# Kernel tuning notes

Hardware: AMD Instinct MI355X
Metric: run time of the kernel (lower is better)

## Reference

```python
import jax, jax.numpy as jnp
import numpy as np

IMG = 224; P = 16; C_IN = 3; D = 768; DEPTH = 12; H = 12; HD = D // H
MLP = 4 * D; NCLS = 1000
GRID = IMG // P; NPATCH = GRID * GRID; N = NPATCH + 1
NRD = (2 * GRID - 1) * (2 * GRID - 1) + 3  # num_relative_distance


def _rel_pos_index():
    # replicates the torch buffer construction (BEiT-style)
    coords = np.stack(np.meshgrid(np.arange(GRID), np.arange(GRID), indexing='ij')).reshape(2, -1)
    rel = (coords[:, :, None] - coords[:, None, :]).transpose(1, 2, 0).astype(np.int64)
    rel[:, :, 0] += GRID - 1
    rel[:, :, 1] += GRID - 1
    rel[:, :, 0] *= 2 * GRID - 1
    idx = np.zeros((N, N), dtype=np.int64)
    idx[1:, 1:] = rel.sum(-1)
    idx[0, :] = NRD - 3
    idx[:, 0] = NRD - 2
    idx[0, 0] = NRD - 1
    return jnp.asarray(idx)

REL_IDX = _rel_pos_index()  # [N, N] int


def setup_inputs() -> dict:
    key = jax.random.key(0)
    ks = jax.random.split(key, 12)
    r = lambda k, shp: jax.random.normal(k, shp, jnp.float32) * 0.02
    return {
        'x': jax.random.normal(ks[0], (32, C_IN, IMG, IMG), jnp.float32),
        'patch_w': r(ks[1], (D, C_IN * P * P)),
        'patch_b': jnp.zeros((D,), jnp.float32),
        'cls_token': r(ks[2], (1, 1, D)),
        'pos_embed': r(ks[3], (1, N, D)),
        'norm1_s': jnp.ones((DEPTH, D), jnp.float32),
        'norm1_b': jnp.zeros((DEPTH, D), jnp.float32),
        'qkv_w': r(ks[4], (DEPTH, 3 * D, D)),
        'q_bias': jnp.zeros((DEPTH, D), jnp.float32),
        'v_bias': jnp.zeros((DEPTH, D), jnp.float32),
        'rpb_table': r(ks[5], (DEPTH, NRD, H)),
        'proj_w': r(ks[6], (DEPTH, D, D)),
        'proj_b': jnp.zeros((DEPTH, D), jnp.float32),
        'norm2_s': jnp.ones((DEPTH, D), jnp.float32),
        'norm2_b': jnp.zeros((DEPTH, D), jnp.float32),
        'fc1_w': r(ks[7], (DEPTH, MLP, D)),
        'fc1_b': jnp.zeros((DEPTH, MLP), jnp.float32),
        'fc2_w': r(ks[8], (DEPTH, D, MLP)),
        'fc2_b': jnp.zeros((DEPTH, D), jnp.float32),
        'gamma1': jnp.full((DEPTH, D), 0.1, jnp.float32),
        'gamma2': jnp.full((DEPTH, D), 0.1, jnp.float32),
        'normf_s': jnp.ones((D,), jnp.float32),
        'normf_b': jnp.zeros((D,), jnp.float32),
        'head_w': r(ks[9], (NCLS, D)),
        'head_b': jnp.zeros((NCLS,), jnp.float32),
    }


def _ln(x, s, b):
    m = jnp.mean(x, -1, keepdims=True)
    v = jnp.mean((x - m) ** 2, -1, keepdims=True)
    return (x - m) * jax.lax.rsqrt(v + 1e-5) * s + b


def reference(x, patch_w, patch_b, cls_token, pos_embed, norm1_s, norm1_b, qkv_w,
              q_bias, v_bias, rpb_table, proj_w, proj_b, norm2_s, norm2_b,
              fc1_w, fc1_b, fc2_w, fc2_b, gamma1, gamma2, normf_s, normf_b,
              head_w, head_b):
    B = x.shape[0]
    # Patch embed: stride=kernel conv == unfold + matmul
    t = x.reshape(B, C_IN, GRID, P, GRID, P).transpose(0, 2, 4, 1, 3, 5).reshape(B, NPATCH, C_IN * P * P)
    t = t @ patch_w.T + patch_b                                   # [B, 196, D]
    t = jnp.concatenate([jnp.broadcast_to(cls_token, (B, 1, D)), t], axis=1) + pos_embed
    scale = HD ** -0.5
    for i in range(DEPTH):
        h = _ln(t, norm1_s[i], norm1_b[i])
        qkv_b = jnp.concatenate([q_bias[i], jnp.zeros_like(q_bias[i]), v_bias[i]])
        qkv = (h @ qkv_w[i].T + qkv_b).reshape(B, N, 3, H, HD)
        q = qkv[:, :, 0].transpose(0, 2, 1, 3)                    # [B, H, N, HD]
        k = qkv[:, :, 1].transpose(0, 2, 1, 3)
        v = qkv[:, :, 2].transpose(0, 2, 1, 3)
        bias = rpb_table[i][REL_IDX].transpose(2, 0, 1)           # [H, N, N]
        attn = jax.nn.softmax(jnp.einsum('bhqd,bhkd->bhqk', q * scale, k) + bias[None], axis=-1)
        o = jnp.einsum('bhqk,bhkd->bhqd', attn, v).transpose(0, 2, 1, 3).reshape(B, N, D)
        t = t + gamma1[i] * (o @ proj_w[i].T + proj_b[i])
        h2 = _ln(t, norm2_s[i], norm2_b[i])
        m = jax.nn.gelu(h2 @ fc1_w[i].T + fc1_b[i], approximate=False) @ fc2_w[i].T + fc2_b[i]
        t = t + gamma2[i] * m
    t = _ln(t, normf_s, normf_b)
    return t[:, 0] @ head_w.T + head_b                            # [B, NCLS]
```

## Files before the change

### kernel.cpp

```cpp
#include <hip/hip_runtime.h>
#include <hip/hip_bf16.h>


typedef __hip_bfloat16 bf16s;
using bf16x8 = __attribute__((ext_vector_type(8))) __bf16;
using f32x4  = __attribute__((ext_vector_type(4))) float;

#define DEV static __device__ __forceinline__

DEV float b2f(bf16s x) { return __bfloat162float(x); }
DEV bf16s f2b(float x) { return __float2bfloat16(x); }

DEV void gload_lds16(const void* g, void* l) {
  __builtin_amdgcn_global_load_lds((const __attribute__((address_space(1))) void*)g,
                                   (__attribute__((address_space(3))) void*)l, 16, 0, 0);
}

constexpr int B_   = 32;
constexpr int H_   = 12;
constexpr int NTOK = 197;
constexpr int NPAD = 224;
constexpr int MVALP= 6272;
constexpr int MVAL = B_*NTOK;
constexpr int MROW = 6400;
constexpr int MLP_ = 3072;
constexpr int BH   = B_*H_;
constexpr int NRD  = 732;
constexpr int NNP  = 7*32*16*14;

constexpr size_t OFF_T   = 0;
constexpr size_t SZ_T    = (size_t)MROW*768*4;
constexpr size_t OFF_H   = OFF_T + SZ_T;
constexpr size_t SZ_H    = (size_t)MROW*768*2;
constexpr size_t OFF_Q   = OFF_H + SZ_H;
constexpr size_t SZ_QKB  = (size_t)BH*NPAD*64*2;
constexpr size_t OFF_K   = OFF_Q + SZ_QKB;
constexpr size_t OFF_VT  = OFF_K + SZ_QKB;
constexpr size_t OFF_P   = OFF_VT + SZ_QKB;
constexpr size_t SZ_P    = (size_t)MROW*MLP_*2;
constexpr size_t OFF_O   = OFF_P + SZ_P;
constexpr size_t OFF_BT  = OFF_O + SZ_H;
constexpr size_t SZ_BT   = (size_t)12*H_*NNP*2;
constexpr size_t OFF_HF  = OFF_BT + SZ_BT;
constexpr size_t OFF_WB  = OFF_HF + 49152;
constexpr size_t WS_NEED = OFF_WB + (size_t)7077888*2;

constexpr size_t WB_QKV = 0;
constexpr size_t WB_PROJ= (size_t)2304*768;
constexpr size_t WB_FC1 = WB_PROJ + (size_t)768*768;
constexpr size_t WB_FC2 = WB_FC1 + (size_t)MLP_*768;

template<int MODE>
__global__ __launch_bounds__(512, 4)
void gemm8p(const bf16s* __restrict__ A, const bf16s* __restrict__ Bw,
            const int K, const int ldc,
            bf16s* __restrict__ Cb,
            const float* __restrict__ e0, const float* __restrict__ e1,
            float* __restrict__ tres,
            bf16s* __restrict__ qp, bf16s* __restrict__ kp, bf16s* __restrict__ vp)
{
  __shared__ bf16s lds[32768];
  const int tid  = threadIdx.x;
  const int lane = tid & 63;
  const int wid  = tid >> 6;
  const int wm   = wid >> 2, wn = wid & 3;

  const int ncols = gridDim.y;
  const int nwg = (int)gridDim.x * ncols;
  const int lin = (int)blockIdx.y * gridDim.x + blockIdx.x;
  const int xcd = lin & 7, pos = lin >> 3;
  const int q8 = nwg >> 3, r8 = nwg & 7;
  const int vid = (xcd < r8) ? xcd*(q8+1) + pos : r8*(q8+1) + (xcd-r8)*q8 + pos;
  constexpr int NBG = (MODE == 0) ? 6 : 8;
  const int gsz = NBG * (int)gridDim.x;
  const int g   = vid / gsz;
  const int rr  = vid - g*gsz;
  const int bm  = rr / NBG;
  const int bn  = g*NBG + (rr - bm*NBG);

  const int srow = (wid << 3) + (lane >> 3);
  const int colg = (((lane & 7) ^ (srow & 7)) << 3);
  const bf16s* gA = A  + (size_t)(bm*128 + srow)*K + colg;
  const bf16s* gB = Bw + (size_t)(bn*128 + srow)*K + colg;
  const size_t rK64 = (size_t)64*K;

  const int r15  = lane & 15;
  const int colr = (lane >> 4) << 3;
  const int exor = (lane & 7) << 3;
  const int ardA = wm*4096 + r15*64;
  const int ardB = 8192 + (wn*32 + r15)*64;

  f32x4 acc[4][2] = {};
  const int J = K >> 7;

#define STGA(h, kt, dbuf) do { \
    const bf16s* _g = gA + (size_t)(h)*rK64 + (size_t)(kt)*64; \
    gload_lds16(_g, &lds[(dbuf)*16384 + (h)*4096 + wid*512 + lane*8]); } while(0)
#define STGB(h, kt, dbuf) do { \
    const bf16s* _g = gB + (size_t)(h)*rK64 + (size_t)(kt)*64; \
    gload_lds16(_g, &lds[(dbuf)*16384 + 8192 + (h)*4096 + wid*512 + lane*8]); } while(0)

  STGB(0,0,0); STGB(1,0,0);
  STGA(0,0,0); STGA(1,0,0);
  STGB(0,1,1); STGB(1,1,1);

  bf16x8 bfr[2][2];

  for (int j = 0; j < J; ++j) {
    const bool more = (j+1 < J);
#pragma unroll
    for (int p = 0; p < 4; ++p) {
      __builtin_amdgcn_sched_barrier(0);
      if (p == 0) {
        asm volatile("s_waitcnt vmcnt(2)" ::: "memory");
      } else if (p == 2) {
        if (j+1 == J) asm volatile("s_waitcnt vmcnt(0)" ::: "memory");
        else          asm volatile("s_waitcnt vmcnt(2)" ::: "memory");
      }
      __builtin_amdgcn_sched_barrier(0);
      __builtin_amdgcn_s_barrier();
      __builtin_amdgcn_sched_barrier(0);

      if (p == 0)      { STGA(0, 2*j+1, 1); STGA(1, 2*j+1, 1); }
      else if (p == 1) { if (more) { STGB(0, 2*j+2, 0); STGB(1, 2*j+2, 0); } }
      else if (p == 2) { if (more) { STGA(0, 2*j+2, 0); STGA(1, 2*j+2, 0); } }
      else             { if (more) { STGB(0, 2*j+3, 1); STGB(1, 2*j+3, 1); } }

      const int d = (p < 2) ? 0 : 1;
      const int dbase = d*16384;
      const int q0 = (p & 1) << 1;
      if ((p & 1) == 0) {
#pragma unroll
        for (int nf=0; nf<2; nf++)
#pragma unroll
          for (int kss=0; kss<2; kss++)
            bfr[nf][kss] = *(const bf16x8*)&lds[dbase + ardB + nf*1024 + (((kss<<5) + colr) ^ exor)];
      }
      bf16x8 a1[2][2];
#pragma unroll
      for (int qq=0; qq<2; qq++)
#pragma unroll
        for (int kss=0; kss<2; kss++)
          a1[qq][kss] = *(const bf16x8*)&lds[dbase + ardA + (q0+qq)*1024 + (((kss<<5) + colr) ^ exor)];
      __builtin_amdgcn_s_setprio(1);
#pragma unroll
      for (int qq=0; qq<2; qq++)
#pragma unroll
        for (int nf=0; nf<2; nf++)
#pragma unroll
          for (int kss=0; kss<2; kss++)
            acc[q0+qq][nf] = __builtin_amdgcn_mfma_f32_16x16x32_bf16(a1[qq][kss], bfr[nf][kss], acc[q0+qq][nf], 0, 0, 0);
      __builtin_amdgcn_s_setprio(0);
    }
  }
#undef STGA
#undef STGB

  const int crow0 = (lane >> 4) * 4;

  if (MODE == 5) {
    __syncthreads();
#pragma unroll
    for (int mf = 0; mf < 4; ++mf)
#pragma unroll
      for (int nf = 0; nf < 2; ++nf)
#pragma unroll
        for (int r = 0; r < 4; ++r) {
          const int lrow = wm*64 + mf*16 + crow0 + r;
          const int lcol = wn*32 + nf*16 + r15;
          const float xx = acc[mf][nf][r] + e0[bn*128 + lcol];
          lds[lrow*136 + lcol] = f2b(0.5f*xx*(1.0f + erff(xx*0.70710678118654752f)));
        }
    __syncthreads();
#pragma unroll
    for (int it = 0; it < 4; ++it) {
      const int sid = it*512 + tid;
      const int row = sid >> 4, cg = sid & 15;
      const int grow = bm*128 + row;
      *(uint4*)&Cb[(size_t)grow*ldc + bn*128 + cg*8] =
          *(const uint4*)&lds[row*136 + cg*8];
    }
    return;
  }

  if (MODE == 0 && bn >= 12) {
    float* lf = (float*)lds;
    __syncthreads();
#pragma unroll
    for (int mf = 0; mf < 4; ++mf)
#pragma unroll
      for (int nf = 0; nf < 2; ++nf)
#pragma unroll
        for (int r = 0; r < 4; ++r) {
          const int col = wn*32 + nf*16 + r15;
          const int row = wm*64 + mf*16 + crow0 + r;
          lf[col*128 + (row ^ (col & 31))] = acc[mf][nf][r];
        }
    __syncthreads();
    const int rem0 = bn*128 - 1536;
#pragma unroll
    for (int ci = 0; ci < 16; ++ci) {
      const int c = wid*16 + ci;
      const int rem = rem0 + c;
      const int hh = rem >> 6, dd = rem & 63;
      const float vb = e1[rem];
      bf16s* vrow = vp + ((size_t)hh*64 + dd)*NPAD;
#pragma unroll
      for (int hf2 = 0; hf2 < 2; ++hf2) {
        const int row = hf2*64 + lane;
        const int grow = bm*128 + row;
        if (grow < MVAL) {
          const int b2 = grow/197, ntok = grow - b2*197;
          vrow[(size_t)b2*H_*64*NPAD + ntok] = f2b(lf[c*128 + (row ^ (c & 31))] + vb);
        }
      }
    }
    return;
  }

  if (MODE == 0) {
    const bool isq = (bn < 6);
    __syncthreads();
#pragma unroll
    for (int mf = 0; mf < 4; ++mf)
#pragma unroll
      for (int nf = 0; nf < 2; ++nf)
#pragma unroll
        for (int r = 0; r < 4; ++r) {
          const int lrow = wm*64 + mf*16 + crow0 + r;
          const int lcol = wn*32 + nf*16 + r15;
          float v = acc[mf][nf][r];
          if (isq) v = (v + e0[bn*128 + lcol])*0.125f;
          lds[lrow*136 + lcol] = f2b(v);
        }
    __syncthreads();
    bf16s* outp = isq ? qp : kp;
#pragma unroll
    for (int it = 0; it < 4; ++it) {
      const int sid = it*512 + tid;
      const int row = sid >> 4, cg = sid & 15;
      const int grow = bm*128 + row;
      if (grow < MVAL) {
        const int bb_ = grow/197, ntok = grow - bb_*197;
        const int lcol = cg*8;
        const int rem = isq ? (bn*128 + lcol) : (bn*128 + lcol - 768);
        const int hh = rem >> 6, dd = rem & 63;
        *(uint4*)&outp[(((size_t)bb_*H_ + hh)*NPAD + ntok)*64 + dd] =
            *(const uint4*)&lds[row*136 + lcol];
      }
    }
  }
}

template<int MODE>
__global__ __launch_bounds__(256, 3)
void gemm64n(const bf16s* __restrict__ A, const bf16s* __restrict__ Bw,
             const int K, const int ldc, bf16s* __restrict__ Cb,
             const float* __restrict__ e0, const float* __restrict__ e1,
             float* __restrict__ tres)
{
  __shared__ bf16s lds[24576];
  const int tid  = threadIdx.x;
  const int lane = tid & 63;
  const int wid  = tid >> 6;
  const int wm   = wid >> 1, wn = wid & 1;

  const int ncols = gridDim.y;
  const int nwg = (int)gridDim.x * ncols;
  const int lin = (int)blockIdx.y * gridDim.x + blockIdx.x;
  const int xcd = lin & 7, pos = lin >> 3;
  const int q8 = nwg >> 3, r8 = nwg & 7;
  const int vid = (xcd < r8) ? xcd*(q8+1) + pos : r8*(q8+1) + (xcd-r8)*q8 + pos;
  const int bm = vid / ncols, bn = vid - bm*ncols;

  const int srow = tid >> 3;
  const int colg = (((tid & 7) ^ (srow & 7)) << 3);
  const bf16s* gA = A  + (size_t)(bm*128 + srow)*K + colg;
  const bf16s* gB = Bw + (size_t)(bn*64  + srow)*K + colg;
  const size_t rK32 = (size_t)32*K;

  const int r15  = lane & 15;
  const int colr = (lane >> 4) << 3;
  const int exor = (lane & 7) << 3;
  const int ardA = wm*4096 + r15*64;
  const int ardB = 8192 + (wn*32 + r15)*64;

  f32x4 acc[4][2] = {};
  const int J = K >> 7;

#define STGA2(h, kt, dbuf) do { \
    const bf16s* _g = gA + (size_t)(h)*rK32 + (size_t)(kt)*64; \
    gload_lds16(_g, &lds[(dbuf)*12288 + (h)*2048 + tid*8]); } while(0)
#define STGB2(h, kt, dbuf) do { \
    const bf16s* _g = gB + (size_t)(h)*rK32 + (size_t)(kt)*64; \
    gload_lds16(_g, &lds[(dbuf)*12288 + 8192 + (h)*2048 + tid*8]); } while(0)

  STGB2(0,0,0); STGB2(1,0,0);
  STGA2(0,0,0); STGA2(1,0,0); STGA2(2,0,0); STGA2(3,0,0);
  STGB2(0,1,1); STGB2(1,1,1);

  bf16x8 bfr[2][2];

  for (int j = 0; j < J; ++j) {
    const bool more = (j+1 < J);
#pragma unroll
    for (int p = 0; p < 4; ++p) {
      __builtin_amdgcn_sched_barrier(0);
      if (p == 0) {
        asm volatile("s_waitcnt vmcnt(2)" ::: "memory");
      } else if (p == 2) {
        if (j+1 == J) asm volatile("s_waitcnt vmcnt(0)" ::: "memory");
        else          asm volatile("s_waitcnt vmcnt(2)" ::: "memory");
      }
      __builtin_amdgcn_sched_barrier(0);
      __builtin_amdgcn_s_barrier();
      __builtin_amdgcn_sched_barrier(0);

      if (p == 0)      { STGA2(0, 2*j+1, 1); STGA2(1, 2*j+1, 1); STGA2(2, 2*j+1, 1); STGA2(3, 2*j+1, 1); }
      else if (p == 1) { if (more) { STGB2(0, 2*j+2, 0); STGB2(1, 2*j+2, 0); } }
      else if (p == 2) { if (more) { STGA2(0, 2*j+2, 0); STGA2(1, 2*j+2, 0); STGA2(2, 2*j+2, 0); STGA2(3, 2*j+2, 0); } }
      else             { if (more) { STGB2(0, 2*j+3, 1); STGB2(1, 2*j+3, 1); } }

      const int d = (p < 2) ? 0 : 1;
      const int dbase = d*12288;
      const int q0 = (p & 1) << 1;
      if ((p & 1) == 0) {
#pragma unroll
        for (int nf=0; nf<2; nf++)
#pragma unroll
          for (int kss=0; kss<2; kss++)
            bfr[nf][kss] = *(const bf16x8*)&lds[dbase + ardB + nf*1024 + (((kss<<5) + colr) ^ exor)];
      }
      bf16x8 a1[2][2];
#pragma unroll
      for (int qq=0; qq<2; qq++)
#pragma unroll
        for (int kss=0; kss<2; kss++)
          a1[qq][kss] = *(const bf16x8*)&lds[dbase + ardA + (q0+qq)*1024 + (((kss<<5) + colr) ^ exor)];
      __builtin_amdgcn_s_setprio(1);
#pragma unroll
      for (int qq=0; qq<2; qq++)
#pragma unroll
        for (int nf=0; nf<2; nf++)
#pragma unroll
          for (int kss=0; kss<2; kss++)
            acc[q0+qq][nf] = __builtin_amdgcn_mfma_f32_16x16x32_bf16(a1[qq][kss], bfr[nf][kss], acc[q0+qq][nf], 0, 0, 0);
      __builtin_amdgcn_s_setprio(0);
    }
  }
#undef STGA2
#undef STGB2

  const int crow0 = (lane >> 4) * 4;
#pragma unroll
  for (int mf = 0; mf < 4; ++mf) {
#pragma unroll
    for (int r = 0; r < 4; ++r) {
      const int grow = bm*128 + wm*64 + mf*16 + crow0 + r;
      {
        float* trow = tres + (size_t)grow*768;
#pragma unroll
        for (int nf = 0; nf < 2; ++nf) {
          const int gcol = bn*64 + wn*32 + nf*16 + r15;
          trow[gcol] += e1[gcol]*(acc[mf][nf][r] + e0[gcol]);
        }
      }
    }
  }
}

__global__ __launch_bounds__(256, 5)
void gemm64p(const bf16s* __restrict__ A, const bf16s* __restrict__ Bw,
             int K,
             const float* __restrict__ e0, const float* __restrict__ e1,
             float* __restrict__ tres)
{
  __shared__ bf16s As[2][64*32];
  __shared__ bf16s Bs[2][128*32];
  const int tid  = threadIdx.x;
  const int lane = tid & 63;
  const int wave = tid >> 6;

  const int ncols = gridDim.y;
  const int nwg = (int)gridDim.x * ncols;
  const int lin = (int)blockIdx.y * gridDim.x + blockIdx.x;
  const int xcd = lin & 7, pos = lin >> 3;
  const int q8 = nwg >> 3, r8 = nwg & 7;
  const int vid = (xcd < r8) ? xcd*(q8+1) + pos : r8*(q8+1) + (xcd-r8)*q8 + pos;
  const int bm = vid / ncols, bn = vid - bm*ncols;

  f32x4 acc[2][4] = {};

  const int sr4  = lane >> 2;
  const int scol = ((lane&3) ^ (sr4&3))*8;
  const bf16s* gA = A  + (size_t)(bm*64  + wave*16 + sr4)*K + scol;
  const bf16s* gB = Bw + (size_t)(bn*128 + wave*32 + sr4)*K + scol;
  const size_t b16 = (size_t)16*K;
  const int dA  = wave*512  + lane*8;
  const int dB0 = wave*1024 + lane*8, dB1 = dB0 + 512;

  const int fr  = lane & 15;
  const int rdk = (((lane>>4) ^ (lane&3)))*8;
  const int wr = wave >> 1, wc = wave & 1;
  const int abase = (wr*32 + fr)*32 + rdk;
  const int bbase = (wc*64 + fr)*32 + rdk;

  const int nk = K >> 5;
  gload_lds16(gA,       &As[0][dA]);
  gload_lds16(gB,       &Bs[0][dB0]);
  gload_lds16(gB + b16, &Bs[0][dB1]);

  int cur = 0;
  for (int kt = 0; kt < nk; ++kt) {
    __syncthreads();
    if (kt + 1 < nk) {
      const bf16s* ga = gA + (size_t)(kt+1)*32;
      const bf16s* gb = gB + (size_t)(kt+1)*32;
      gload_lds16(ga,       &As[cur^1][dA]);
      gload_lds16(gb,       &Bs[cur^1][dB0]);
      gload_lds16(gb + b16, &Bs[cur^1][dB1]);
    }
    bf16x8 af[2], bfr[4];
    af[0] = *(const bf16x8*)&As[cur][abase];
    af[1] = *(const bf16x8*)&As[cur][abase + 512];
#pragma unroll
    for (int n2=0;n2<4;n2++) bfr[n2] = *(const bf16x8*)&Bs[cur][bbase + n2*512];
#pragma unroll
    for (int m=0;m<2;m++)
#pragma unroll
      for (int n2=0;n2<4;n2++)
        acc[m][n2] = __builtin_amdgcn_mfma_f32_16x16x32_bf16(af[m], bfr[n2], acc[m][n2], 0, 0, 0);
    cur ^= 1;
  }

  const int crow0 = (lane>>4)*4;
#pragma unroll
  for (int m=0;m<2;m++) {
#pragma unroll
    for (int r=0;r<4;r++) {
      const int grow = bm*64 + wr*32 + m*16 + crow0 + r;
      if (grow >= MVALP) continue;
      const int bb_ = grow/196, p = grow - bb_*196;
      float* trow = tres + ((size_t)bb_*197 + 1 + p)*768;
      const float* prow = e1 + (size_t)(1+p)*768;
#pragma unroll
      for (int n2=0;n2<4;n2++) {
        const int gcol = bn*128 + wc*64 + n2*16 + fr;
        trow[gcol] = acc[m][n2][r] + e0[gcol] + prow[gcol];
      }
    }
  }
}

__global__ __launch_bounds__(256)
void f2b_k(const float* __restrict__ src, bf16s* __restrict__ dst, int n4)
{
  int id = blockIdx.x*256 + threadIdx.x;
  if (id >= n4) return;
  const float4 v = ((const float4*)src)[id];
  union { bf16s b[4]; uint2 u; } uu;
  uu.b[0] = f2b(v.x); uu.b[1] = f2b(v.y); uu.b[2] = f2b(v.z); uu.b[3] = f2b(v.w);
  ((uint2*)dst)[id] = uu.u;
}

__global__ __launch_bounds__(256)
void prep_k(const float* __restrict__ tin, const float* __restrict__ s,
            const float* __restrict__ b, bf16s* __restrict__ outp,
            const float* __restrict__ qw, const float* __restrict__ pw,
            const float* __restrict__ f1, const float* __restrict__ f2,
            bf16s* __restrict__ wb)
{
  const int tid = threadIdx.x;
  if (blockIdx.x < MVAL) {
    const int r = blockIdx.x;
    const float* xr = tin + (size_t)r*768;
    float v0 = xr[tid], v1 = xr[tid+256], v2 = xr[tid+512];
    float sum = v0+v1+v2;
#pragma unroll
    for (int off=32; off>=1; off>>=1) sum += __shfl_xor(sum, off, 64);
    __shared__ float red[8];
    const int wv = tid>>6, ln = tid&63;
    if (ln==0) red[wv] = sum;
    __syncthreads();
    const float mean = (red[0]+red[1]+red[2]+red[3]) * (1.0f/768.0f);
    const float d0=v0-mean, d1=v1-mean, d2=v2-mean;
    float sq = d0*d0 + d1*d1 + d2*d2;
#pragma unroll
    for (int off=32; off>=1; off>>=1) sq += __shfl_xor(sq, off, 64);
    if (ln==0) red[4+wv] = sq;
    __syncthreads();
    const float rs = rsqrtf((red[4]+red[5]+red[6]+red[7])*(1.0f/768.0f) + 1e-5f);
    bf16s* orow = outp + (size_t)r*768;
    orow[tid]     = f2b(d0*rs*s[tid]     + b[tid]);
    orow[tid+256] = f2b(d1*rs*s[tid+256] + b[tid+256]);
    orow[tid+512] = f2b(d2*rs*s[tid+512] + b[tid+512]);
  } else {
    int id = (blockIdx.x - MVAL)*256 + tid;
    const float* src; size_t dst; int loc;
    if (id < 442368)           { src = qw; loc = id;          dst = WB_QKV; }
    else if (id < 589824)      { src = pw; loc = id-442368;   dst = WB_PROJ; }
    else if (id < 1179648)     { src = f1; loc = id-589824;   dst = WB_FC1; }
    else                       { src = f2; loc = id-1179648;  dst = WB_FC2; }
    const float4 v = ((const float4*)src)[loc];
    union { bf16s bb[4]; uint2 u; } uu;
    uu.bb[0] = f2b(v.x); uu.bb[1] = f2b(v.y); uu.bb[2] = f2b(v.z); uu.bb[3] = f2b(v.w);
    ((uint2*)(wb + dst))[loc] = uu.u;
  }
}

__global__ __launch_bounds__(256)
void bias_all_k(const float* __restrict__ rpb, bf16s* __restrict__ biasT)
{
  int id = blockIdx.x*256 + threadIdx.x;
  if (id >= 12*H_*NNP) return;
  const int l   = id / (H_*NNP);
  const int r2  = id - l*(H_*NNP);
  const int hh  = r2 / NNP;
  const int rem = r2 - hh*NNP;
  const int qt   = rem / 7168;
  const int idx2 = rem - qt*7168;
  const int lrow = idx2 / 224;
  const int idx3 = idx2 - lrow*224;
  const int fr   = idx3 / 14;
  const int nt   = idx3 - fr*14;
  int i = qt*32 + lrow;
  int j = nt*16 + fr;
  if (i > 196) i = 196;
  if (j > 196) j = 196;
  int v;
  if (i==0 && j==0)      v = NRD-1;
  else if (i==0)         v = NRD-3;
  else if (j==0)         v = NRD-2;
  else {
    const int p = i-1, q = j-1;
    v = (p/14 - q/14 + 13)*27 + (p%14 - q%14 + 13);
  }
  biasT[id] = f2b(rpb[(size_t)l*NRD*H_ + v*H_ + hh]);
}

__global__ __launch_bounds__(256)
void im2col_k(const float* __restrict__ x, bf16s* __restrict__ pat)
{
  int id = blockIdx.x*256 + threadIdx.x;
  if (id >= MVALP*768) return;
  int col = id % 768;  int row = id / 768;
  int b = row / 196, p = row % 196;
  int gy = p / 14, gx = p % 14;
  int c = col >> 8, rem = col & 255, py = rem >> 4, px = rem & 15;
  pat[id] = f2b(x[ ((size_t)(b*3 + c)*224 + gy*16 + py)*224 + gx*16 + px ]);
}

__global__ __launch_bounds__(256)
void clspos_k(const float* __restrict__ cls, const float* __restrict__ pos, float* __restrict__ t)
{
  int id = blockIdx.x*256 + threadIdx.x;
  int d = id % 768, b = id / 768;
  t[(size_t)b*197*768 + d] = cls[d] + pos[d];
}

__global__ __launch_bounds__(256)
void ln_k(const float* __restrict__ tin, const float* __restrict__ s,
          const float* __restrict__ b, bf16s* __restrict__ outp, int instride)
{
  const int r = blockIdx.x, tid = threadIdx.x;
  const float* xr = tin + (size_t)r*instride;
  float v0 = xr[tid], v1 = xr[tid+256], v2 = xr[tid+512];
  float sum = v0+v1+v2;
#pragma unroll
  for (int off=32; off>=1; off>>=1) sum += __shfl_xor(sum, off, 64);
  __shared__ float red[8];
  const int wv = tid>>6, ln = tid&63;
  if (ln==0) red[wv] = sum;
  __syncthreads();
  const float mean = (red[0]+red[1]+red[2]+red[3]) * (1.0f/768.0f);
  const float d0=v0-mean, d1=v1-mean, d2=v2-mean;
  float sq = d0*d0 + d1*d1 + d2*d2;
#pragma unroll
  for (int off=32; off>=1; off>>=1) sq += __shfl_xor(sq, off, 64);
  if (ln==0) red[4+wv] = sq;
  __syncthreads();
  const float rs = rsqrtf((red[4]+red[5]+red[6]+red[7])*(1.0f/768.0f) + 1e-5f);
  bf16s* orow = outp + (size_t)r*768;
  orow[tid]     = f2b(d0*rs*s[tid]     + b[tid]);
  orow[tid+256] = f2b(d1*rs*s[tid+256] + b[tid+256]);
  orow[tid+512] = f2b(d2*rs*s[tid+512] + b[tid+512]);
}

__global__ __launch_bounds__(64)
void attn_fused(const bf16s* __restrict__ q, const bf16s* __restrict__ k,
                const bf16s* __restrict__ vT, const bf16s* __restrict__ biasT,
                bf16s* __restrict__ o)
{
  __shared__ bf16s Pl[32][232];
  bf16s* Plf = &Pl[0][0];
  const int gid = blockIdx.x;
  const int qt = gid % 7, bh = gid / 7;
  const int b = bh / H_, hh = bh % H_;
  const int lane = threadIdx.x;
  const int fr = lane & 15, fk = (lane>>4)*8;
  const int g4 = (lane >> 4) * 4;

  const bf16s* bTq = biasT + (size_t)hh*NNP + (size_t)qt*7168;
#pragma unroll
  for (int it = 0; it < 14; ++it)
    gload_lds16(bTq + it*512 + lane*8, &Plf[it*512 + lane*8]);

  const bf16s* qp = q + (size_t)bh*NPAD*64;
  const bf16s* kp = k + (size_t)bh*NPAD*64;
  bf16x8 a[2][2];
#pragma unroll
  for (int m=0;m<2;m++)
#pragma unroll
    for (int kk=0;kk<2;kk++)
      a[m][kk] = *(const bf16x8*)&qp[(qt*32 + m*16 + fr)*64 + kk*32 + fk];

  f32x4 acc[2][13] = {};
  __builtin_amdgcn_s_setprio(1);
#pragma unroll
  for (int nt=0; nt<13; nt++) {
    bf16x8 bb0 = *(const bf16x8*)&kp[(nt*16 + fr)*64 + fk];
    bf16x8 bb1 = *(const bf16x8*)&kp[(nt*16 + fr)*64 + 32 + fk];
    acc[0][nt] = __builtin_amdgcn_mfma_f32_16x16x32_bf16(a[0][0], bb0, acc[0][nt], 0,0,0);
    acc[0][nt] = __builtin_amdgcn_mfma_f32_16x16x32_bf16(a[0][1], bb1, acc[0][nt], 0,0,0);
    acc[1][nt] = __builtin_amdgcn_mfma_f32_16x16x32_bf16(a[1][0], bb0, acc[1][nt], 0,0,0);
    acc[1][nt] = __builtin_amdgcn_mfma_f32_16x16x32_bf16(a[1][1], bb1, acc[1][nt], 0,0,0);
  }
  __builtin_amdgcn_s_setprio(0);

  asm volatile("s_waitcnt vmcnt(0)" ::: "memory");
  __builtin_amdgcn_sched_barrier(0);

  const uint* Plu = (const uint*)Plf;
  const bf16s zb = f2b(0.0f);

#pragma unroll
  for (int mm = 0; mm < 2; ++mm) {
    const int m = 1 - mm;
    uint br[4][7];
#pragma unroll
    for (int r2 = 0; r2 < 4; ++r2) {
      const int lrow = m*16 + g4 + r2;
      const int ub = (lrow*224 + fr*14) >> 1;
#pragma unroll
      for (int j = 0; j < 7; ++j) br[r2][j] = Plu[ub + j];
    }
#pragma unroll
    for (int r2 = 0; r2 < 4; ++r2) {
      const int lrow = m*16 + g4 + r2;
      const int row = qt*32 + lrow;
      if (row < NTOK) {
        float s[13]; float mx = -3.0e38f;
#pragma unroll
        for (int nt = 0; nt < 12; ++nt) {
          const uint u = br[r2][nt >> 1];
          const uint bb = (nt & 1) ? (u & 0xffff0000u) : (u << 16);
          const float v = acc[m][nt][r2] + __uint_as_float(bb);
          s[nt] = v;
          mx = fmaxf(mx, v);
        }
        {
          const uint u = br[r2][6];
          const float v = acc[m][12][r2] + __uint_as_float(u << 16);
          s[12] = v;
          if (fr < 5) mx = fmaxf(mx, v);
        }
        mx = fmaxf(mx, __shfl_xor(mx, 1, 64));
        mx = fmaxf(mx, __shfl_xor(mx, 2, 64));
        mx = fmaxf(mx, __shfl_xor(mx, 4, 64));
        mx = fmaxf(mx, __shfl_xor(mx, 8, 64));
        float sum = 0.f;
#pragma unroll
        for (int nt = 0; nt < 12; ++nt) {
          const float p = __expf(s[nt] - mx);
          s[nt] = p; sum += p;
        }
        {
          const float p = (fr < 5) ? __expf(s[12] - mx) : 0.0f;
          s[12] = p; sum += p;
        }
        sum += __shfl_xor(sum, 1, 64);
        sum += __shfl_xor(sum, 2, 64);
        sum += __shfl_xor(sum, 4, 64);
        sum += __shfl_xor(sum, 8, 64);
        const float inv = 1.0f / sum;
#pragma unroll
        for (int nt = 0; nt < 13; ++nt)
          Pl[lrow][nt*16 + fr] = f2b(s[nt]*inv);
        Pl[lrow][208 + fr] = zb;
      } else {
#pragma unroll
        for (int nt = 0; nt < 14; ++nt)
          Pl[lrow][nt*16 + fr] = zb;
      }
    }
  }

  __syncthreads();

  const bf16s* Vp = vT + (size_t)bh*64*NPAD;
  f32x4 pacc[2][4] = {};
  __builtin_amdgcn_s_setprio(1);
  for (int kt=0; kt<7; kt++) {
    bf16x8 a0 = *(const bf16x8*)&Pl[fr][kt*32 + fk];
    bf16x8 a1 = *(const bf16x8*)&Pl[16 + fr][kt*32 + fk];
#pragma unroll
    for (int nf=0;nf<4;nf++) {
      bf16x8 bb = *(const bf16x8*)&Vp[(size_t)(nf*16 + fr)*NPAD + kt*32 + fk];
      pacc[0][nf] = __builtin_amdgcn_mfma_f32_16x16x32_bf16(a0, bb, pacc[0][nf], 0,0,0);
      pacc[1][nf] = __builtin_amdgcn_mfma_f32_16x16x32_bf16(a1, bb, pacc[1][nf], 0,0,0);
    }
  }
  __builtin_amdgcn_s_setprio(0);

  __syncthreads();
#pragma unroll
  for (int m=0;m<2;m++)
#pragma unroll
    for (int nf=0;nf<4;nf++)
#pragma unroll
      for (int r2=0;r2<4;r2++)
        Pl[m*16 + (lane>>4)*4 + r2][nf*16 + fr] = f2b(pacc[m][nf][r2]);
  __syncthreads();
  bf16s* obase = o + ((size_t)b*NTOK + qt*32)*768 + hh*64;
#pragma unroll
  for (int it=0; it<8; ++it) {
    const int id = it*64 + lane;
    const int row = id >> 4, c4 = (id & 15)*4;
    if (qt*32 + row < NTOK) {
      union { bf16s bb[4]; uint2 u; } uu;
      uu.bb[0]=Pl[row][c4]; uu.bb[1]=Pl[row][c4+1]; uu.bb[2]=Pl[row][c4+2]; uu.bb[3]=Pl[row][c4+3];
      *(uint2*)&obase[(size_t)row*768 + c4] = uu.u;
    }
  }
}

__global__ __launch_bounds__(256)
void head_k(const bf16s* __restrict__ hf, const float* __restrict__ hw,
            const float* __restrict__ hb, float* __restrict__ outp)
{
  const int b = blockIdx.y;
  const int n = blockIdx.x*256 + threadIdx.x;
  __shared__ float xs[768];
  for (int i=threadIdx.x; i<768; i+=256) xs[i] = b2f(hf[b*768+i]);
  __syncthreads();
  if (n < 1000) {
    const float* wr = hw + (size_t)n*768;
    float acc2 = hb[n];
    for (int k2=0;k2<768;k2++) acc2 += xs[k2]*wr[k2];
    outp[b*1000 + n] = acc2;
  }
}

extern "C" void kernel_launch(void* const* d_in, const int* in_sizes, int n_in,
                              void* d_out, int out_size, void* d_ws, size_t ws_size,
                              hipStream_t stream)
{
  const float* x       = (const float*)d_in[0];
  const float* patch_w = (const float*)d_in[1];
  const float* patch_b = (const float*)d_in[2];
  const float* cls_tok = (const float*)d_in[3];
  const float* pos_emb = (const float*)d_in[4];
  const float* norm1_s = (const float*)d_in[5];
  const float* norm1_b = (const float*)d_in[6];
  const float* qkv_w   = (const float*)d_in[7];
  const float* q_bias  = (const float*)d_in[8];
  const float* v_bias  = (const float*)d_in[9];
  const float* rpb     = (const float*)d_in[10];
  const float* proj_w  = (const float*)d_in[11];
  const float* proj_b  = (const float*)d_in[12];
  const float* norm2_s = (const float*)d_in[13];
  const float* norm2_b = (const float*)d_in[14];
  const float* fc1_w   = (const float*)d_in[15];
  const float* fc1_b   = (const float*)d_in[16];
  const float* fc2_w   = (const float*)d_in[17];
  const float* fc2_b   = (const float*)d_in[18];
  const float* gamma1  = (const float*)d_in[19];
  const float* gamma2  = (const float*)d_in[20];
  const float* normf_s = (const float*)d_in[21];
  const float* normf_b = (const float*)d_in[22];
  const float* head_w  = (const float*)d_in[23];
  const float* head_b  = (const float*)d_in[24];
  float* out = (float*)d_out;

  char* w = (char*)d_ws;
  float* t    = (float*)(w + OFF_T);
  bf16s* h    = (bf16s*)(w + OFF_H);
  bf16s* qb   = (bf16s*)(w + OFF_Q);
  bf16s* kb   = (bf16s*)(w + OFF_K);
  bf16s* vT   = (bf16s*)(w + OFF_VT);
  bf16s* m1   = (bf16s*)(w + OFF_P);
  bf16s* pat  = (bf16s*)(w + OFF_P);
  bf16s* o    = (bf16s*)(w + OFF_O);
  bf16s* biasT= (bf16s*)(w + OFF_BT);
  bf16s* hf   = (bf16s*)(w + OFF_HF);
  bf16s* wb   = (bf16s*)(w + OFF_WB);
  (void)ws_size; (void)in_sizes; (void)n_in; (void)out_size; (void)WS_NEED;

  hipMemsetAsync(h  + (size_t)MVAL*768,  0, (size_t)(MROW-MVAL)*768*2,  stream);
  hipMemsetAsync(o  + (size_t)MVAL*768,  0, (size_t)(MROW-MVAL)*768*2,  stream);
  hipMemsetAsync(m1 + (size_t)MVAL*MLP_, 0, (size_t)(MROW-MVAL)*MLP_*2, stream);
  hipMemsetAsync(qb, 0, SZ_QKB, stream);
  hipMemsetAsync(kb, 0, SZ_QKB, stream);
  hipMemsetAsync(vT, 0, SZ_QKB, stream);

  bias_all_k<<<(12*H_*NNP + 255)/256, 256, 0, stream>>>(rpb, biasT);
  im2col_k<<<(MVALP*768)/256, 256, 0, stream>>>(x, pat);
  clspos_k<<<96, 256, 0, stream>>>(cls_tok, pos_emb, t);
  f2b_k<<<(768*768/4)/256, 256, 0, stream>>>(patch_w, wb, 768*768/4);
  gemm64p<<<dim3(98,6), 256, 0, stream>>>(pat, wb, 768, patch_b, pos_emb, t);

  for (int l = 0; l < 12; ++l) {
    prep_k<<<MVAL + 6912, 256, 0, stream>>>(t, norm1_s + l*768, norm1_b + l*768, h,
                                            qkv_w + (size_t)l*2304*768, proj_w + (size_t)l*768*768,
                                            fc1_w + (size_t)l*MLP_*768, fc2_w + (size_t)l*768*MLP_, wb);
    gemm8p<0><<<dim3(50,18), 512, 0, stream>>>(h, wb + WB_QKV, 768, 2304, nullptr,
                                               q_bias + l*768, v_bias + l*768, nullptr,
                                               qb, kb, vT);
    attn_fused<<<BH*7, 64, 0, stream>>>(qb, kb, vT, biasT + (size_t)l*H_*NNP, o);
    gemm64n<2><<<dim3(50,12), 256, 0, stream>>>(o, wb + WB_PROJ, 768, 0, nullptr,
                                                proj_b + l*768, gamma1 + l*768, t);
    ln_k<<<MVAL, 256, 0, stream>>>(t, norm2_s + l*768, norm2_b + l*768, h, 768);
    gemm8p<5><<<dim3(50,24), 512, 0, stream>>>(h, wb + WB_FC1, 768, MLP_, m1,
                                               fc1_b + l*MLP_, nullptr, nullptr,
                                               nullptr, nullptr, nullptr);
    gemm64n<4><<<dim3(50,12), 256, 0, stream>>>(m1, wb + WB_FC2, 3072, 0, nullptr,
                                                fc2_b + l*768, gamma2 + l*768, t);
  }

  ln_k<<<32, 256, 0, stream>>>(t, normf_s, normf_b, hf, 197*768);
  head_k<<<dim3(4,32), 256, 0, stream>>>(hf, head_w, head_b, out);
}
```

Before: 2.702 ms.

## Hoist per-layer weight conversion into one upfront kernel for all layers

Replaces the per-layer prep kernel, which fused LN1 with fp32-to-bf16 weight conversion, with a single wconv_k launch that converts all 12 layers' weights into a larger workspace before the loop. LN1 now uses the plain ln_k. It also drops the memsets of the q and k buffers and changes the block-index mapping for the fc2 GEMM to be column-major. Conversion becomes one large bandwidth-bound launch, at the cost of a bigger workspace and relying on the padding in q/k no longer needing zeroing.

```diff
diff --git a/kernel.cpp b/kernel.cpp
--- a/kernel.cpp
+++ b/kernel.cpp
@@ -27,6 +27,7 @@
 constexpr int BH   = B_*H_;
 constexpr int NRD  = 732;
 constexpr int NNP  = 7*32*16*14;
+constexpr size_t WBL = 7077888;
 
 constexpr size_t OFF_T   = 0;
 constexpr size_t SZ_T    = (size_t)MROW*768*4;
@@ -43,7 +44,7 @@
 constexpr size_t SZ_BT   = (size_t)12*H_*NNP*2;
 constexpr size_t OFF_HF  = OFF_BT + SZ_BT;
 constexpr size_t OFF_WB  = OFF_HF + 49152;
-constexpr size_t WS_NEED = OFF_WB + (size_t)7077888*2;
+constexpr size_t WS_NEED = OFF_WB + (size_t)13*WBL*2;
 
 constexpr size_t WB_QKV = 0;
 constexpr size_t WB_PROJ= (size_t)2304*768;
@@ -271,7 +272,9 @@
   const int xcd = lin & 7, pos = lin >> 3;
   const int q8 = nwg >> 3, r8 = nwg & 7;
   const int vid = (xcd < r8) ? xcd*(q8+1) + pos : r8*(q8+1) + (xcd-r8)*q8 + pos;
-  const int bm = vid / ncols, bn = vid - bm*ncols;
+  int bm, bn;
+  if (MODE == 4) { bn = vid / (int)gridDim.x; bm = vid - bn*(int)gridDim.x; }
+  else           { bm = vid / ncols;          bn = vid - bm*ncols; }
 
   const int srow = tid >> 3;
   const int colg = (((tid & 7) ^ (srow & 7)) << 3);
@@ -464,48 +467,22 @@
 }
 
 __global__ __launch_bounds__(256)
-void prep_k(const float* __restrict__ tin, const float* __restrict__ s,
-            const float* __restrict__ b, bf16s* __restrict__ outp,
-            const float* __restrict__ qw, const float* __restrict__ pw,
-            const float* __restrict__ f1, const float* __restrict__ f2,
-            bf16s* __restrict__ wb)
-{
-  const int tid = threadIdx.x;
-  if (blockIdx.x < MVAL) {
-    const int r = blockIdx.x;
-    const float* xr = tin + (size_t)r*768;
-    float v0 = xr[tid], v1 = xr[tid+256], v2 = xr[tid+512];
-    float sum = v0+v1+v2;
-#pragma unroll
-    for (int off=32; off>=1; off>>=1) sum += __shfl_xor(sum, off, 64);
-    __shared__ float red[8];
-    const int wv = tid>>6, ln = tid&63;
-    if (ln==0) red[wv] = sum;
-    __syncthreads();
-    const float mean = (red[0]+red[1]+red[2]+red[3]) * (1.0f/768.0f);
-    const float d0=v0-mean, d1=v1-mean, d2=v2-mean;
-    float sq = d0*d0 + d1*d1 + d2*d2;
-#pragma unroll
-    for (int off=32; off>=1; off>>=1) sq += __shfl_xor(sq, off, 64);
-    if (ln==0) red[4+wv] = sq;
-    __syncthreads();
-    const float rs = rsqrtf((red[4]+red[5]+red[6]+red[7])*(1.0f/768.0f) + 1e-5f);
-    bf16s* orow = outp + (size_t)r*768;
-    orow[tid]     = f2b(d0*rs*s[tid]     + b[tid]);
-    orow[tid+256] = f2b(d1*rs*s[tid+256] + b[tid+256]);
-    orow[tid+512] = f2b(d2*rs*s[tid+512] + b[tid+512]);
-  } else {
-    int id = (blockIdx.x - MVAL)*256 + tid;
-    const float* src; size_t dst; int loc;
-    if (id < 442368)           { src = qw; loc = id;          dst = WB_QKV; }
-    else if (id < 589824)      { src = pw; loc = id-442368;   dst = WB_PROJ; }
-    else if (id < 1179648)     { src = f1; loc = id-589824;   dst = WB_FC1; }
-    else                       { src = f2; loc = id-1179648;  dst = WB_FC2; }
-    const float4 v = ((const float4*)src)[loc];
-    union { bf16s bb[4]; uint2 u; } uu;
-    uu.bb[0] = f2b(v.x); uu.bb[1] = f2b(v.y); uu.bb[2] = f2b(v.z); uu.bb[3] = f2b(v.w);
-    ((uint2*)(wb + dst))[loc] = uu.u;
-  }
+void wconv_k(const float* __restrict__ qw, const float* __restrict__ pw,
+             const float* __restrict__ f1, const float* __restrict__ f2,
+             bf16s* __restrict__ wb)
+{
+  const int id = blockIdx.x*256 + threadIdx.x;
+  const int l = id / 1769472;
+  const int r = id - l*1769472;
+  const float* src; size_t dst; int loc;
+  if (r < 442368)       { src = qw + (size_t)l*1769472; loc = r;          dst = WB_QKV; }
+  else if (r < 589824)  { src = pw + (size_t)l*589824;  loc = r-442368;   dst = WB_PROJ; }
+  else if (r < 1179648) { src = f1 + (size_t)l*2359296; loc = r-589824;   dst = WB_FC1; }
+  else                  { src = f2 + (size_t)l*2359296; loc = r-1179648;  dst = WB_FC2; }
+  const float4 v = ((const float4*)src)[loc];
+  union { bf16s bb[4]; uint2 u; } uu;
+  uu.bb[0] = f2b(v.x); uu.bb[1] = f2b(v.y); uu.bb[2] = f2b(v.z); uu.bb[3] = f2b(v.w);
+  ((uint2*)(wb + (size_t)l*WBL + dst))[loc] = uu.u;
 }
 
 __global__ __launch_bounds__(256)
@@ -794,36 +771,35 @@
   bf16s* biasT= (bf16s*)(w + OFF_BT);
   bf16s* hf   = (bf16s*)(w + OFF_HF);
   bf16s* wb   = (bf16s*)(w + OFF_WB);
+  bf16s* wbp  = wb + (size_t)12*WBL;
   (void)ws_size; (void)in_sizes; (void)n_in; (void)out_size; (void)WS_NEED;
 
   hipMemsetAsync(h  + (size_t)MVAL*768,  0, (size_t)(MROW-MVAL)*768*2,  stream);
   hipMemsetAsync(o  + (size_t)MVAL*768,  0, (size_t)(MROW-MVAL)*768*2,  stream);
   hipMemsetAsync(m1 + (size_t)MVAL*MLP_, 0, (size_t)(MROW-MVAL)*MLP_*2, stream);
-  hipMemsetAsync(qb, 0, SZ_QKB, stream);
-  hipMemsetAsync(kb, 0, SZ_QKB, stream);
   hipMemsetAsync(vT, 0, SZ_QKB, stream);
 
+  wconv_k<<<82944, 256, 0, stream>>>(qkv_w, proj_w, fc1_w, fc2_w, wb);
   bias_all_k<<<(12*H_*NNP + 255)/256, 256, 0, stream>>>(rpb, biasT);
   im2col_k<<<(MVALP*768)/256, 256, 0, stream>>>(x, pat);
   clspos_k<<<96, 256, 0, stream>>>(cls_tok, pos_emb, t);
-  f2b_k<<<(768*768/4)/256, 256, 0, stream>>>(patch_w, wb, 768*768/4);
-  gemm64p<<<dim3(98,6), 256, 0, stream>>>(pat, wb, 768, patch_b, pos_emb, t);
+  f2b_k<<<(768*768/4)/256, 256, 0, stream>>>(patch_w, wbp, 768*768/4);
+  gemm64p<<<dim3(98,6), 256, 0, stream>>>(pat, wbp, 768, patch_b, pos_emb, t);
 
   for (int l = 0; l < 12; ++l) {
-    prep_k<<<MVAL + 6912, 256, 0, stream>>>(t, norm1_s + l*768, norm1_b + l*768, h,
-                                            qkv_w + (size_t)l*2304*768, proj_w + (size_t)l*768*768,
-                                            fc1_w + (size_t)l*MLP_*768, fc2_w + (size_t)l*768*MLP_, wb);
-    gemm8p<0><<<dim3(50,18), 512, 0, stream>>>(h, wb + WB_QKV, 768, 2304, nullptr,
+    bf16s* wbl = wb + (size_t)l*WBL;
+    ln_k<<<MVAL, 256, 0, stream>>>(t, norm1_s + l*768, norm1_b + l*768, h, 768);
+    gemm8p<0><<<dim3(50,18), 512, 0, stream>>>(h, wbl + WB_QKV, 768, 2304, nullptr,
                                                q_bias + l*768, v_bias + l*768, nullptr,
                                                qb, kb, vT);
     attn_fused<<<BH*7, 64, 0, stream>>>(qb, kb, vT, biasT + (size_t)l*H_*NNP, o);
-    gemm64n<2><<<dim3(50,12), 256, 0, stream>>>(o, wb + WB_PROJ, 768, 0, nullptr,
+    gemm64n<2><<<dim3(50,12), 256, 0, stream>>>(o, wbl + WB_PROJ, 768, 0, nullptr,
                                                 proj_b + l*768, gamma1 + l*768, t);
     ln_k<<<MVAL, 256, 0, stream>>>(t, norm2_s + l*768, norm2_b + l*768, h, 768);
-    gemm8p<5><<<dim3(50,24), 512, 0, stream>>>(h, wb + WB_FC1, 768, MLP_, m1,
+    gemm8p<5><<<dim3(50,24), 512, 0, stream>>>(h, wbl + WB_FC1, 768, MLP_, m1,
                                                fc1_b + l*MLP_, nullptr, nullptr,
                                                nullptr, nullptr, nullptr);
-    gemm64n<4><<<dim3(50,12), 256, 0, stream>>>(m1, wb + WB_FC2, 3072, 0, nullptr,
+    gemm64n<4><<<dim3(50,12), 256, 0, stream>>>(m1, wbl + WB_FC2, 3072, 0, nullptr,
                                                 fc2_b + l*768, gamma2 + l*768, t);
   }
 
```

New measurement: 2.981 ms. 1.1x slower.
